# Optimization experiments

Hardware: AMD Instinct MI355X
Metric: run time of the kernel (lower is better)

Reference implementation:

```python
import jax, jax.numpy as jnp
import numpy as np

N, T, D, H = 32, 1024, 1152, 16
DH = D // H            # 72
MLP = int(D * 4.0)     # 4608
EPS = 1e-6


def setup_inputs() -> dict:
    key = jax.random.key(0)
    ks = jax.random.split(key, 14)
    s = 0.02
    return {
        "x": jax.random.normal(ks[0], (N, T, D), jnp.float32),
        "c": jax.random.normal(ks[1], (N, D), jnp.float32),
        "qkv_w": jax.random.normal(ks[2], (D, 3 * D), jnp.float32) * s,
        "qkv_b": jax.random.normal(ks[3], (3 * D,), jnp.float32) * s,
        "proj_w": jax.random.normal(ks[4], (D, D), jnp.float32) * s,
        "proj_b": jax.random.normal(ks[5], (D,), jnp.float32) * s,
        "fc1_w": jax.random.normal(ks[6], (D, MLP), jnp.float32) * s,
        "fc1_b": jax.random.normal(ks[7], (MLP,), jnp.float32) * s,
        "fc2_w": jax.random.normal(ks[8], (MLP, D), jnp.float32) * s,
        "fc2_b": jax.random.normal(ks[9], (D,), jnp.float32) * s,
        "ada_w": jax.random.normal(ks[10], (D, 6 * D), jnp.float32) * s,
        "ada_b": jax.random.normal(ks[11], (6 * D,), jnp.float32) * s,
    }


def _layernorm(x):
    m = jnp.mean(x, axis=-1, keepdims=True)
    v = jnp.var(x, axis=-1, keepdims=True)
    return (x - m) * jax.lax.rsqrt(v + EPS)


def _modulate(x, shift, scale):
    # shift, scale: (N, D) broadcast over T
    return x * (1.0 + scale[:, None, :]) + shift[:, None, :]


def _attention(x, qkv_w, qkv_b, proj_w, proj_b):
    n, t, d = x.shape
    scale = DH ** (-0.5)
    qkv = x @ qkv_w + qkv_b                       # (N,T,3D)
    qkv = qkv.reshape(n, t, 3, H, DH)
    q, k, v = qkv[:, :, 0], qkv[:, :, 1], qkv[:, :, 2]  # each (N,T,H,DH)
    # Faithful to source: matmul over the LAST two dims -> per-token
    # head-vs-head attention of shape (N,T,H,H), softmax over heads.
    attn = jnp.einsum("nthd,ntkd->nthk", q * scale, k)
    attn = jax.nn.softmax(attn, axis=-1)
    out = jnp.einsum("nthk,ntkd->nthd", attn, v)  # (N,T,H,DH)
    out = out.transpose(0, 2, 1, 3).reshape(n, t, d)  # faithful scramble
    return out @ proj_w + proj_b


def _mlp(x, fc1_w, fc1_b, fc2_w, fc2_b):
    h = jax.nn.gelu(x @ fc1_w + fc1_b, approximate=False)  # exact GELU (torch default)
    return h @ fc2_w + fc2_b


def reference(x, c, qkv_w, qkv_b, proj_w, proj_b, fc1_w, fc1_b, fc2_w, fc2_b,
              ada_w, ada_b):
    ada = jax.nn.silu(c) @ ada_w + ada_b          # (N, 6D)
    (shift_msa, scale_msa, gate_msa,
     shift_mlp, scale_mlp, gate_mlp) = jnp.split(ada, 6, axis=1)
    x = x + gate_msa[:, None, :] * _attention(
        _modulate(_layernorm(x), shift_msa, scale_msa),
        qkv_w, qkv_b, proj_w, proj_b)
    x = x + gate_mlp[:, None, :] * _mlp(
        _modulate(_layernorm(x), shift_mlp, scale_mlp),
        fc1_w, fc1_b, fc2_w, fc2_b)
    return x
```

## Files before the change

### kernel.cpp

```cpp
#include <hip/hip_runtime.h>

#define DEV __device__ __forceinline__

typedef __attribute__((ext_vector_type(8))) short short8;
typedef __attribute__((ext_vector_type(8))) __bf16 bf16x8;
typedef __attribute__((ext_vector_type(4))) float f32x4;

#define TD      1024
#define DD      1152
#define DHH     72
#define MLPD    4608
#define QKVN    3456
#define ADAN    6912
#define MROWS   32768

DEV unsigned short f32_to_bf16(float f) {
  unsigned int u = __float_as_uint(f);
  u += 0x7fffu + ((u >> 16) & 1u);
  return (unsigned short)(u >> 16);
}

DEV void gl16(const void* g, void* l) {
  __builtin_amdgcn_global_load_lds((__attribute__((address_space(1))) void*)g,
                                   (__attribute__((address_space(3))) void*)l,
                                   16, 0, 0);
}

DEV bf16x8 zero_bf16x8() {
  short8 z = {0, 0, 0, 0, 0, 0, 0, 0};
  return __builtin_bit_cast(bf16x8, z);
}

DEV float gelu_exact(float v) {
  return 0.5f * v * (1.0f + erff(v * 0.70710678118654752f));
}

#define WAITV(n) asm volatile("s_waitcnt vmcnt(" #n ")" ::: "memory")

__global__ __launch_bounds__(256) void wtrans_frag(const float* __restrict__ W,
                                                   unsigned short* __restrict__ Bp,
                                                   int K, int N) {
  const int nb = blockIdx.x * 32, kb = blockIdx.y * 32;
  const int tx = threadIdx.x, ty = threadIdx.y;
  const size_t K16 = (size_t)K << 4;
  #pragma unroll
  for (int i = 0; i < 4; ++i) {
    const int k = kb + ty + i * 8;
    const int n = nb + tx;
    const unsigned short v = f32_to_bf16(W[(size_t)k * N + n]);
    Bp[(size_t)(n >> 4) * K16 + (size_t)(k >> 5) * 512 +
       (size_t)(((n & 15) + ((k >> 3) & 3) * 16) * 8 + (k & 7))] = v;
  }
}

__global__ __launch_bounds__(256) void ada_kernel(const float* __restrict__ c,
                                                  const float* __restrict__ ada_w,
                                                  const float* __restrict__ ada_b,
                                                  float* __restrict__ ada_out) {
  __shared__ float sc[DD];
  const int n = blockIdx.y;
  const int col = blockIdx.x * 256 + threadIdx.x;
  for (int i = threadIdx.x; i < DD; i += 256) {
    float v = c[(size_t)n * DD + i];
    sc[i] = v / (1.0f + __expf(-v));
  }
  __syncthreads();
  float acc = ada_b[col];
  #pragma unroll 8
  for (int k = 0; k < DD; ++k)
    acc += sc[k] * ada_w[(size_t)k * ADAN + col];
  ada_out[(size_t)n * ADAN + col] = acc;
}

__global__ __launch_bounds__(256) void ln_mod_kernel(const float* __restrict__ X,
                                                     const float* __restrict__ ada,
                                                     int soff,
                                                     unsigned short* __restrict__ out) {
  const int row = blockIdx.x;
  const int batch = row >> 10;
  const float* xr = X + (size_t)row * DD;
  const int t = threadIdx.x;

  float4 v0 = reinterpret_cast<const float4*>(xr)[t];
  float4 v1 = make_float4(0.f, 0.f, 0.f, 0.f);
  const bool has2 = (t < 32);
  if (has2) v1 = reinterpret_cast<const float4*>(xr)[256 + t];

  float s  = v0.x + v0.y + v0.z + v0.w + v1.x + v1.y + v1.z + v1.w;
  float sq = v0.x*v0.x + v0.y*v0.y + v0.z*v0.z + v0.w*v0.w
           + v1.x*v1.x + v1.y*v1.y + v1.z*v1.z + v1.w*v1.w;
  #pragma unroll
  for (int m = 1; m < 64; m <<= 1) {
    s  += __shfl_xor(s, m);
    sq += __shfl_xor(sq, m);
  }
  __shared__ float red[8];
  const int wv = t >> 6;
  if ((t & 63) == 0) { red[wv] = s; red[4 + wv] = sq; }
  __syncthreads();
  s  = red[0] + red[1] + red[2] + red[3];
  sq = red[4] + red[5] + red[6] + red[7];
  const float mean = s * (1.0f / 1152.0f);
  const float var  = sq * (1.0f / 1152.0f) - mean * mean;
  const float rstd = rsqrtf(var + 1e-6f);

  const float* shp = ada + (size_t)batch * ADAN + soff;
  const float* scp = shp + DD;
  unsigned short* orow = out + (size_t)row * DD;

  {
    const int col = t * 4;
    ushort4 o4;
    o4.x = f32_to_bf16((v0.x - mean) * rstd * (1.0f + scp[col + 0]) + shp[col + 0]);
    o4.y = f32_to_bf16((v0.y - mean) * rstd * (1.0f + scp[col + 1]) + shp[col + 1]);
    o4.z = f32_to_bf16((v0.z - mean) * rstd * (1.0f + scp[col + 2]) + shp[col + 2]);
    o4.w = f32_to_bf16((v0.w - mean) * rstd * (1.0f + scp[col + 3]) + shp[col + 3]);
    reinterpret_cast<ushort4*>(orow)[t] = o4;
  }
  if (has2) {
    const int col = 1024 + t * 4;
    ushort4 o4;
    o4.x = f32_to_bf16((v1.x - mean) * rstd * (1.0f + scp[col + 0]) + shp[col + 0]);
    o4.y = f32_to_bf16((v1.y - mean) * rstd * (1.0f + scp[col + 1]) + shp[col + 1]);
    o4.z = f32_to_bf16((v1.z - mean) * rstd * (1.0f + scp[col + 2]) + shp[col + 2]);
    o4.w = f32_to_bf16((v1.w - mean) * rstd * (1.0f + scp[col + 3]) + shp[col + 3]);
    reinterpret_cast<ushort4*>(orow)[256 + t] = o4;
  }
}

template <int EPI>
__global__ __launch_bounds__(512) void gemmB(
    const unsigned short* __restrict__ A, const unsigned short* __restrict__ Bp,
    const float* __restrict__ bias, const float* __restrict__ ada, int ada_off,
    const float* __restrict__ resid, unsigned short* __restrict__ out_bf,
    float* __restrict__ out_f, int N, int K, int ntn) {
  __shared__ unsigned short lds[32768];
  const int tid = threadIdx.x;
  const int lane = tid & 63, w = tid >> 6;
  const int wm = w >> 2, wn = w & 3;
  const int l15 = lane & 15, lg = lane >> 4;

  const int nwg = 128 * ntn, cpx = nwg >> 3;
  const int wg = (blockIdx.x & 7) * cpx + (blockIdx.x >> 3);
  const int bm = wg / ntn, bn = wg - bm * ntn;

  const unsigned short* __restrict__ Ag = A + (size_t)bm * 256 * K;
  const size_t K16 = (size_t)K << 4;
  const unsigned short* __restrict__ Bgl = Bp + (size_t)(bn * 16 + wn * 2) * K16 + lane * 8;

  const int rp0 = tid >> 3;
  const int ch0 = ((tid & 7) ^ (rp0 & 7)) * 8;

#define STG_A(BUFS, KT) do {                                                              \
    gl16(Ag + (size_t)(rp0) * K + (size_t)(KT) * 64 + ch0, &lds[(BUFS) + tid * 8]);       \
    gl16(Ag + (size_t)(rp0 + 64) * K + (size_t)(KT) * 64 + ch0,                           \
         &lds[(BUFS) + 4096 + tid * 8]);                                                  \
    gl16(Ag + (size_t)(rp0 + 128) * K + (size_t)(KT) * 64 + ch0,                          \
         &lds[(BUFS) + 8192 + tid * 8]);                                                  \
    gl16(Ag + (size_t)(rp0 + 192) * K + (size_t)(KT) * 64 + ch0,                          \
         &lds[(BUFS) + 12288 + tid * 8]);                                                 \
  } while (0)

#define LOAD_B(DST, KT) do {                                                              \
    _Pragma("unroll") for (int nq_ = 0; nq_ < 2; ++nq_)                                   \
      _Pragma("unroll") for (int nf_ = 0; nf_ < 2; ++nf_)                                 \
        _Pragma("unroll") for (int kb_ = 0; kb_ < 2; ++kb_)                               \
          DST[nq_][nf_][kb_] = *(const bf16x8*)&Bgl[(size_t)(nq_ * 8 + nf_) * K16 +       \
                                                    ((KT) * 2 + kb_) * 512];              \
  } while (0)

  const int chA0 = (lg ^ (l15 & 7)) * 8;
  const int chA1 = chA0 ^ 32;
  const int arow0 = wm * 64 + l15;

  f32x4 acc[2][2][4][2];
  #pragma unroll
  for (int a = 0; a < 2; ++a)
    #pragma unroll
    for (int b = 0; b < 2; ++b)
      #pragma unroll
      for (int m = 0; m < 4; ++m)
        #pragma unroll
        for (int n2 = 0; n2 < 2; ++n2)
          acc[a][b][m][n2] = (f32x4){0.f, 0.f, 0.f, 0.f};

#define SUBPH(MQ, KB, BSET) do {                                                          \
    bf16x8 af_[4];                                                                        \
    _Pragma("unroll") for (int mf_ = 0; mf_ < 4; ++mf_)                                   \
      af_[mf_] = *(const bf16x8*)&lb[(arow0 + (MQ) * 128 + mf_ * 16) * 64 +               \
                                     ((KB) ? chA1 : chA0)];                               \
    __builtin_amdgcn_s_setprio(1);                                                        \
    _Pragma("unroll") for (int mf_ = 0; mf_ < 4; ++mf_)                                   \
      _Pragma("unroll") for (int nq_ = 0; nq_ < 2; ++nq_)                                 \
        _Pragma("unroll") for (int nf_ = 0; nf_ < 2; ++nf_)                               \
          acc[MQ][nq_][mf_][nf_] = __builtin_amdgcn_mfma_f32_16x16x32_bf16(               \
              af_[mf_], BSET[nq_][nf_][KB], acc[MQ][nq_][mf_][nf_], 0, 0, 0);             \
    __builtin_amdgcn_s_setprio(0);                                                        \
  } while (0)

#define TILE(T, BCUR, BNXT) do {                                                          \
    const unsigned short* lb = lds + (((T) & 1) << 14);                                   \
    STG_A((((T) + 1) & 1) << 14, (T) + 1);                                                \
    LOAD_B(BNXT, (T) + 1);                                                                \
    SUBPH(0, 0, BCUR);                                                                    \
    SUBPH(0, 1, BCUR);                                                                    \
    SUBPH(1, 0, BCUR);                                                                    \
    SUBPH(1, 1, BCUR);                                                                    \
    WAITV(0);                                                                             \
    __builtin_amdgcn_s_barrier();                                                         \
  } while (0)

  const int NT = K >> 6;

  bf16x8 BX[2][2][2], BY[2][2][2];

  STG_A(0, 0);
  LOAD_B(BX, 0);
  WAITV(0);
  __builtin_amdgcn_s_barrier();

  for (int t = 0; t < NT - 2; t += 2) {
    TILE(t, BX, BY);
    TILE(t + 1, BY, BX);
  }
  TILE(NT - 2, BX, BY);
  {
    const unsigned short* lb = lds + (((NT - 1) & 1) << 14);
    SUBPH(0, 0, BY);
    SUBPH(0, 1, BY);
    SUBPH(1, 0, BY);
    SUBPH(1, 1, BY);
  }
#undef STG_A
#undef LOAD_B
#undef SUBPH
#undef TILE

  const int batch = bm >> 2;
  #pragma unroll
  for (int nq = 0; nq < 2; ++nq) {
    const int colbase = bn * 256 + nq * 128 + wn * 32;
    if (colbase >= N) continue;
    #pragma unroll
    for (int nf = 0; nf < 2; ++nf) {
      const int colg = colbase + nf * 16 + l15;
      const float bv = bias[colg];
      float g2 = 0.0f;
      if constexpr (EPI == 1 || EPI == 3) g2 = ada[(size_t)batch * ADAN + ada_off + colg];
      #pragma unroll
      for (int mq = 0; mq < 2; ++mq) {
        #pragma unroll
        for (int mf = 0; mf < 4; ++mf) {
          #pragma unroll
          for (int r = 0; r < 4; ++r) {
            const size_t row = (size_t)bm * 256 + wm * 64 + mq * 128 + mf * 16 + lg * 4 + r;
            const size_t idx = row * (size_t)N + colg;
            const float v = acc[mq][nq][mf][nf][r] + bv;
            if constexpr (EPI == 0)      out_bf[idx] = f32_to_bf16(v);
            else if constexpr (EPI == 2) out_bf[idx] = f32_to_bf16(gelu_exact(v));
            else if constexpr (EPI == 1) out_f[idx] = resid[idx] + g2 * v;
            else                         out_f[idx] = out_f[idx] + g2 * v;
          }
        }
      }
    }
  }
}

__global__ __launch_bounds__(256) void attn_kernel(const unsigned short* __restrict__ qkv,
                                                   unsigned short* __restrict__ y) {
  const int tid = threadIdx.x, w = tid >> 6, lane = tid & 63;
  const int l15 = lane & 15, lg = lane >> 4;
  const int tok = blockIdx.x * 4 + w;
  const int n = tok >> 10, t = tok & 1023;

  __shared__ unsigned short Pl[4][16 * 32];
  __shared__ unsigned short Vl[4][16 * 80];

  for (int i = lane; i < 16 * 32; i += 64)
    if ((i & 31) >= 16) Pl[w][i] = 0;

  const size_t rowb = (size_t)tok * QKVN;
  const float scale = 0.11785113019775793f;

  bf16x8 aq[3];
  #pragma unroll
  for (int kk = 0; kk < 3; ++kk) {
    const int d0 = kk * 32 + lg * 8;
    aq[kk] = (d0 < DHH) ? *(const bf16x8*)&qkv[rowb + l15 * DHH + d0] : zero_bf16x8();
  }

  for (int c = lane; c < 144; c += 64) {
    const int r = c / 9, cc = (c % 9) * 8;
    *(short8*)&Vl[w][r * 80 + cc] = *(const short8*)&qkv[rowb + 2 * DD + r * DHH + cc];
  }

  f32x4 s = (f32x4){0.f, 0.f, 0.f, 0.f};
  #pragma unroll
  for (int kk = 0; kk < 3; ++kk) {
    const int d0 = kk * 32 + lg * 8;
    bf16x8 bk = (d0 < DHH) ? *(const bf16x8*)&qkv[rowb + DD + l15 * DHH + d0] : zero_bf16x8();
    s = __builtin_amdgcn_mfma_f32_16x16x32_bf16(aq[kk], bk, s, 0, 0, 0);
  }

  float p[4], mx[4], ssum[4];
  #pragma unroll
  for (int r = 0; r < 4; ++r) { p[r] = s[r] * scale; mx[r] = p[r]; }
  #pragma unroll
  for (int mk = 1; mk <= 8; mk <<= 1)
    #pragma unroll
    for (int r = 0; r < 4; ++r) mx[r] = fmaxf(mx[r], __shfl_xor(mx[r], mk));
  #pragma unroll
  for (int r = 0; r < 4; ++r) { p[r] = __expf(p[r] - mx[r]); ssum[r] = p[r]; }
  #pragma unroll
  for (int mk = 1; mk <= 8; mk <<= 1)
    #pragma unroll
    for (int r = 0; r < 4; ++r) ssum[r] += __shfl_xor(ssum[r], mk);

  #pragma unroll
  for (int r = 0; r < 4; ++r)
    Pl[w][(lg * 4 + r) * 32 + l15] = f32_to_bf16(p[r] / ssum[r]);

  bf16x8 pa = *(const bf16x8*)&Pl[w][l15 * 32 + lg * 8];
  const int kb = (lg & 1) * 8;
  f32x4 o[5];
  #pragma unroll
  for (int df = 0; df < 5; ++df) {
    short8 bvv;
    #pragma unroll
    for (int j = 0; j < 8; ++j)
      bvv[j] = (short)Vl[w][(kb + j) * 80 + df * 16 + l15];
    o[df] = __builtin_amdgcn_mfma_f32_16x16x32_bf16(
        pa, __builtin_bit_cast(bf16x8, bvv), (f32x4){0.f, 0.f, 0.f, 0.f}, 0, 0, 0);
  }

  unsigned short* yb = y + (size_t)n * (TD * DD);
  #pragma unroll
  for (int df = 0; df < 5; ++df) {
    const int d = df * 16 + l15;
    if (d < DHH) {
      #pragma unroll
      for (int r = 0; r < 4; ++r) {
        const int h = lg * 4 + r;
        yb[h * 73728 + t * DHH + d] = f32_to_bf16(o[df][r]);
      }
    }
  }
}

extern "C" void kernel_launch(void* const* d_in, const int* in_sizes, int n_in,
                              void* d_out, int out_size, void* d_ws, size_t ws_size,
                              hipStream_t stream) {
  (void)in_sizes; (void)n_in; (void)out_size; (void)ws_size;
  const float* x      = (const float*)d_in[0];
  const float* c      = (const float*)d_in[1];
  const float* qkv_w  = (const float*)d_in[2];
  const float* qkv_b  = (const float*)d_in[3];
  const float* proj_w = (const float*)d_in[4];
  const float* proj_b = (const float*)d_in[5];
  const float* fc1_w  = (const float*)d_in[6];
  const float* fc1_b  = (const float*)d_in[7];
  const float* fc2_w  = (const float*)d_in[8];
  const float* fc2_b  = (const float*)d_in[9];
  const float* ada_w  = (const float*)d_in[10];
  const float* ada_b  = (const float*)d_in[11];
  float* out = (float*)d_out;

  char* ws = (char*)d_ws;
  unsigned short* hbuf    = (unsigned short*)ws;
  unsigned short* qkvbuf  = hbuf;
  unsigned short* attnbuf = hbuf + (size_t)MROWS * QKVN;
  size_t off = 301989888ull;
  unsigned short* xm    = (unsigned short*)(ws + off); off += 75497472ull;
  unsigned short* wtq   = (unsigned short*)(ws + off); off += (size_t)3584 * DD * 2;
  unsigned short* wtp   = (unsigned short*)(ws + off); off += (size_t)1280 * DD * 2;
  unsigned short* wtf1  = (unsigned short*)(ws + off); off += (size_t)4608 * DD * 2;
  unsigned short* wtf2  = (unsigned short*)(ws + off); off += (size_t)1280 * MLPD * 2;
  float*          adab  = (float*)(ws + off); off += 884736ull;

  const dim3 tb(32, 8);
  hipLaunchKernelGGL(wtrans_frag, dim3(QKVN / 32, DD / 32), tb, 0, stream, qkv_w, wtq, DD, QKVN);
  hipLaunchKernelGGL(wtrans_frag, dim3(DD / 32, DD / 32),   tb, 0, stream, proj_w, wtp, DD, DD);
  hipLaunchKernelGGL(wtrans_frag, dim3(MLPD / 32, DD / 32), tb, 0, stream, fc1_w, wtf1, DD, MLPD);
  hipLaunchKernelGGL(wtrans_frag, dim3(DD / 32, MLPD / 32), tb, 0, stream, fc2_w, wtf2, MLPD, DD);

  hipLaunchKernelGGL(ada_kernel, dim3(ADAN / 256, 32), dim3(256), 0, stream, c, ada_w, ada_b, adab);

  hipLaunchKernelGGL(ln_mod_kernel, dim3(MROWS), dim3(256), 0, stream, x, adab, 0, xm);

  hipLaunchKernelGGL((gemmB<0>), dim3(128 * 14), dim3(512), 0, stream,
                     xm, wtq, qkv_b, nullptr, 0, nullptr, qkvbuf, nullptr, QKVN, DD, 14);

  hipLaunchKernelGGL(attn_kernel, dim3(MROWS / 4), dim3(256), 0, stream, qkvbuf, attnbuf);

  hipLaunchKernelGGL((gemmB<1>), dim3(128 * 5), dim3(512), 0, stream,
                     attnbuf, wtp, proj_b, adab, 2304, x, nullptr, out, DD, DD, 5);

  hipLaunchKernelGGL(ln_mod_kernel, dim3(MROWS), dim3(256), 0, stream, out, adab, 3456, xm);

  hipLaunchKernelGGL((gemmB<2>), dim3(128 * 18), dim3(512), 0, stream,
                     xm, wtf1, fc1_b, nullptr, 0, nullptr, hbuf, nullptr, MLPD, DD, 18);

  hipLaunchKernelGGL((gemmB<3>), dim3(128 * 5), dim3(512), 0, stream,
                     hbuf, wtf2, fc2_b, adab, 5760, nullptr, nullptr, out, DD, MLPD, 5);
}
```

Before: 2.001 ms.

## Use 256x128 tile GEMM with plain transposed weights for QKV and proj

New measurement: 1.846 ms. 1.08x faster.

```diff
diff --git a/kernel.cpp b/kernel.cpp
--- a/kernel.cpp
+++ b/kernel.cpp
@@ -36,6 +36,21 @@
 }
 
 #define WAITV(n) asm volatile("s_waitcnt vmcnt(" #n ")" ::: "memory")
+
+__global__ __launch_bounds__(256) void wtrans_kernel(const float* __restrict__ W,
+                                                     unsigned short* __restrict__ Wt,
+                                                     int K, int N) {
+  __shared__ unsigned short tile[32][33];
+  const int nb = blockIdx.x * 32, kb = blockIdx.y * 32;
+  const int tx = threadIdx.x, ty = threadIdx.y;
+  #pragma unroll
+  for (int i = ty; i < 32; i += 8)
+    tile[i][tx] = f32_to_bf16(W[(size_t)(kb + i) * N + nb + tx]);
+  __syncthreads();
+  #pragma unroll
+  for (int i = ty; i < 32; i += 8)
+    Wt[(size_t)(nb + i) * K + kb + tx] = tile[tx][i];
+}
 
 __global__ __launch_bounds__(256) void wtrans_frag(const float* __restrict__ W,
                                                    unsigned short* __restrict__ Bp,
@@ -189,13 +204,11 @@
     _Pragma("unroll") for (int mf_ = 0; mf_ < 4; ++mf_)                                   \
       af_[mf_] = *(const bf16x8*)&lb[(arow0 + (MQ) * 128 + mf_ * 16) * 64 +               \
                                      ((KB) ? chA1 : chA0)];                               \
-    __builtin_amdgcn_s_setprio(1);                                                        \
     _Pragma("unroll") for (int mf_ = 0; mf_ < 4; ++mf_)                                   \
       _Pragma("unroll") for (int nq_ = 0; nq_ < 2; ++nq_)                                 \
         _Pragma("unroll") for (int nf_ = 0; nf_ < 2; ++nf_)                               \
           acc[MQ][nq_][mf_][nf_] = __builtin_amdgcn_mfma_f32_16x16x32_bf16(               \
               af_[mf_], BSET[nq_][nf_][KB], acc[MQ][nq_][mf_][nf_], 0, 0, 0);             \
-    __builtin_amdgcn_s_setprio(0);                                                        \
   } while (0)
 
 #define TILE(T, BCUR, BNXT) do {                                                          \
@@ -206,7 +219,7 @@
     SUBPH(0, 1, BCUR);                                                                    \
     SUBPH(1, 0, BCUR);                                                                    \
     SUBPH(1, 1, BCUR);                                                                    \
-    WAITV(0);                                                                             \
+    WAITV(8);          \
     __builtin_amdgcn_s_barrier();                                                         \
   } while (0)
 
@@ -216,7 +229,7 @@
 
   STG_A(0, 0);
   LOAD_B(BX, 0);
-  WAITV(0);
+  WAITV(8);
   __builtin_amdgcn_s_barrier();
 
   for (int t = 0; t < NT - 2; t += 2) {
@@ -267,6 +280,101 @@
   }
 }
 
+template <int EPI>
+__global__ __launch_bounds__(512) void gemm3b(
+    const unsigned short* __restrict__ A, const unsigned short* __restrict__ Bt,
+    const float* __restrict__ bias, const float* __restrict__ ada, int ada_off,
+    const float* __restrict__ resid, unsigned short* __restrict__ out_bf,
+    float* __restrict__ out_f, int N, int K, int ntn) {
+  __shared__ unsigned short lds[24576];
+  const int tid = threadIdx.x;
+  const int lane = tid & 63, w = tid >> 6;
+  const int wm = w >> 1, wn = w & 1;
+  const int l15 = lane & 15, lg = lane >> 4;
+
+  const int nwg = 128 * ntn, cpx = nwg >> 3;
+  const int wg = (blockIdx.x & 7) * cpx + (blockIdx.x >> 3);
+  const int bm = wg / ntn, bn = wg - bm * ntn;
+
+  const unsigned short* __restrict__ Ag = A + (size_t)bm * 256 * K;
+  const unsigned short* __restrict__ Bg = Bt + (size_t)bn * 128 * K;
+
+  const int srow = tid >> 2;
+  const int gch = ((tid & 3) ^ ((tid >> 3) & 3)) * 8;
+
+#define STG(SL, KT) do {                                                                 \
+    gl16(Ag + (size_t)srow * K + (size_t)(KT) * 32 + gch, &lds[(SL) + tid * 8]);         \
+    gl16(Ag + (size_t)(srow + 128) * K + (size_t)(KT) * 32 + gch,                        \
+         &lds[(SL) + 4096 + tid * 8]);                                                   \
+    gl16(Bg + (size_t)srow * K + (size_t)(KT) * 32 + gch,                                \
+         &lds[(SL) + 8192 + tid * 8]);                                                   \
+  } while (0)
+
+  const int chA = (lg ^ ((l15 >> 1) & 3)) * 8;
+  const int arow0 = wm * 64 + l15;
+  const int brow0 = wn * 64 + l15;
+
+  f32x4 acc[4][4];
+  #pragma unroll
+  for (int m = 0; m < 4; ++m)
+    #pragma unroll
+    for (int nn = 0; nn < 4; ++nn)
+      acc[m][nn] = (f32x4){0.f, 0.f, 0.f, 0.f};
+
+  const int NT = K >> 5;
+
+  STG(0, 0);
+  for (int t = 0; t < NT; ++t) {
+    const int sl = (t & 1) * 12288, ns = sl ^ 12288;
+    if (t + 1 < NT) {
+      STG(ns, t + 1);
+      WAITV(3);
+    } else {
+      WAITV(0);
+    }
+    __builtin_amdgcn_s_barrier();
+
+    const unsigned short* lb = lds + sl;
+    bf16x8 af[4], bfv[4];
+    #pragma unroll
+    for (int mf = 0; mf < 4; ++mf)
+      af[mf] = *(const bf16x8*)&lb[(arow0 + mf * 16) * 32 + chA];
+    #pragma unroll
+    for (int nf = 0; nf < 4; ++nf)
+      bfv[nf] = *(const bf16x8*)&lb[8192 + (brow0 + nf * 16) * 32 + chA];
+    #pragma unroll
+    for (int mf = 0; mf < 4; ++mf)
+      #pragma unroll
+      for (int nf = 0; nf < 4; ++nf)
+        acc[mf][nf] = __builtin_amdgcn_mfma_f32_16x16x32_bf16(af[mf], bfv[nf], acc[mf][nf], 0, 0, 0);
+    __builtin_amdgcn_s_barrier();
+  }
+#undef STG
+
+  const int batch = bm >> 2;
+  const size_t row0 = (size_t)bm * 256 + wm * 64;
+  const int col0 = bn * 128 + wn * 64;
+  #pragma unroll
+  for (int nf = 0; nf < 4; ++nf) {
+    const int colg = col0 + nf * 16 + l15;
+    const float bv = bias[colg];
+    float g2 = 0.0f;
+    if constexpr (EPI == 1 || EPI == 3) g2 = ada[(size_t)batch * ADAN + ada_off + colg];
+    #pragma unroll
+    for (int mf = 0; mf < 4; ++mf) {
+      #pragma unroll
+      for (int r = 0; r < 4; ++r) {
+        const size_t idx = (row0 + mf * 16 + lg * 4 + r) * (size_t)N + colg;
+        const float v = acc[mf][nf][r] + bv;
+        if constexpr (EPI == 0)      out_bf[idx] = f32_to_bf16(v);
+        else if constexpr (EPI == 2) out_bf[idx] = f32_to_bf16(gelu_exact(v));
+        else if constexpr (EPI == 1) out_f[idx] = resid[idx] + g2 * v;
+        else                         out_f[idx] = out_f[idx] + g2 * v;
+      }
+    }
+  }
+}
+
 __global__ __launch_bounds__(256) void attn_kernel(const unsigned short* __restrict__ qkv,
                                                    unsigned short* __restrict__ y) {
   const int tid = threadIdx.x, w = tid >> 6, lane = tid & 63;
@@ -372,29 +480,29 @@
   unsigned short* attnbuf = hbuf + (size_t)MROWS * QKVN;
   size_t off = 301989888ull;
   unsigned short* xm    = (unsigned short*)(ws + off); off += 75497472ull;
-  unsigned short* wtq   = (unsigned short*)(ws + off); off += (size_t)3584 * DD * 2;
-  unsigned short* wtp   = (unsigned short*)(ws + off); off += (size_t)1280 * DD * 2;
-  unsigned short* wtf1  = (unsigned short*)(ws + off); off += (size_t)4608 * DD * 2;
+  unsigned short* wtq   = (unsigned short*)(ws + off); off += (size_t)QKVN * DD * 2;
+  unsigned short* wtp   = (unsigned short*)(ws + off); off += (size_t)DD * DD * 2;
+  unsigned short* wtf1  = (unsigned short*)(ws + off); off += (size_t)MLPD * DD * 2;
   unsigned short* wtf2  = (unsigned short*)(ws + off); off += (size_t)1280 * MLPD * 2;
   float*          adab  = (float*)(ws + off); off += 884736ull;
 
   const dim3 tb(32, 8);
-  hipLaunchKernelGGL(wtrans_frag, dim3(QKVN / 32, DD / 32), tb, 0, stream, qkv_w, wtq, DD, QKVN);
-  hipLaunchKernelGGL(wtrans_frag, dim3(DD / 32, DD / 32),   tb, 0, stream, proj_w, wtp, DD, DD);
-  hipLaunchKernelGGL(wtrans_frag, dim3(MLPD / 32, DD / 32), tb, 0, stream, fc1_w, wtf1, DD, MLPD);
-  hipLaunchKernelGGL(wtrans_frag, dim3(DD / 32, MLPD / 32), tb, 0, stream, fc2_w, wtf2, MLPD, DD);
+  hipLaunchKernelGGL(wtrans_kernel, dim3(QKVN / 32, DD / 32), tb, 0, stream, qkv_w, wtq, DD, QKVN);
+  hipLaunchKernelGGL(wtrans_kernel, dim3(DD / 32, DD / 32),   tb, 0, stream, proj_w, wtp, DD, DD);
+  hipLaunchKernelGGL(wtrans_frag,   dim3(MLPD / 32, DD / 32), tb, 0, stream, fc1_w, wtf1, DD, MLPD);
+  hipLaunchKernelGGL(wtrans_frag,   dim3(DD / 32, MLPD / 32), tb, 0, stream, fc2_w, wtf2, MLPD, DD);
 
   hipLaunchKernelGGL(ada_kernel, dim3(ADAN / 256, 32), dim3(256), 0, stream, c, ada_w, ada_b, adab);
 
   hipLaunchKernelGGL(ln_mod_kernel, dim3(MROWS), dim3(256), 0, stream, x, adab, 0, xm);
 
-  hipLaunchKernelGGL((gemmB<0>), dim3(128 * 14), dim3(512), 0, stream,
-                     xm, wtq, qkv_b, nullptr, 0, nullptr, qkvbuf, nullptr, QKVN, DD, 14);
+  hipLaunchKernelGGL((gemm3b<0>), dim3(128 * 27), dim3(512), 0, stream,
+                     xm, wtq, qkv_b, nullptr, 0, nullptr, qkvbuf, nullptr, QKVN, DD, 27);
 
   hipLaunchKernelGGL(attn_kernel, dim3(MROWS / 4), dim3(256), 0, stream, qkvbuf, attnbuf);
 
-  hipLaunchKernelGGL((gemmB<1>), dim3(128 * 5), dim3(512), 0, stream,
-                     attnbuf, wtp, proj_b, adab, 2304, x, nullptr, out, DD, DD, 5);
+  hipLaunchKernelGGL((gemm3b<1>), dim3(128 * 9), dim3(512), 0, stream,
+                     attnbuf, wtp, proj_b, adab, 2304, x, nullptr, out, DD, DD, 9);
 
   hipLaunchKernelGGL(ln_mod_kernel, dim3(MROWS), dim3(256), 0, stream, out, adab, 3456, xm);
 
```
